# Kernel optimization log

Hardware: AMD Instinct MI355X
Metric: run time of the kernel (lower is better)

The kernel has to match this reference:

```python
import jax, jax.numpy as jnp
import numpy as np

PAD = 0  # padding token id; its embedding row is zero (padding_idx)


def setup_inputs() -> dict:
    key = jax.random.key(0)
    k1, k2, k3 = jax.random.split(key, 3)
    HOPS, VOCAB, D = 3, 50257, 128
    B, M, S = 32, 512, 6        # batch, memory slots, tokens per slot
    T, L = 128, 64              # trees per example, tokens per (flattened) tree
    # hop+1 embedding tables, normal(0, 0.1) like the torch init
    C = 0.1 * jax.random.normal(k1, (HOPS + 1, VOCAB, D), dtype=jnp.float32)
    C = C.at[:, PAD].set(0.0)   # padding_idx row = 0
    story = jax.random.randint(k2, (B, M, S), 0, VOCAB, dtype=jnp.int32)
    kb_tokens = jax.random.randint(k3, (B, T, L), 0, VOCAB, dtype=jnp.int32)
    return {"C": C, "story": story, "kb_tokens": kb_tokens}


def reference(C, story, kb_tokens):
    # C: [hops+1, V, D]; story: [B, M, S]; kb_tokens: [B, T, L]
    hops = C.shape[0] - 1
    B = story.shape[0]
    D = C.shape[-1]
    u = jnp.zeros((B, D), dtype=C.dtype)
    for hop in range(hops):
        # key memory: story slots (sum over tokens) + tree memories (sum over
        # all subtree tokens == dfs recursive sum, since PAD embeds to zero)
        m_story_A = jnp.take(C[hop], story, axis=0).sum(axis=2)       # [B,M,D]
        tree_A = jnp.take(C[hop], kb_tokens, axis=0).sum(axis=2)      # [B,T,D]
        m_A = jnp.concatenate([m_story_A, tree_A], axis=1)            # [B,M+T,D]
        prob = jax.nn.softmax(jnp.einsum("bmd,bd->bm", m_A, u), axis=1)
        # value memory with next-hop table
        m_story_C = jnp.take(C[hop + 1], story, axis=0).sum(axis=2)
        tree_C = jnp.take(C[hop + 1], kb_tokens, axis=0).sum(axis=2)
        m_C = jnp.concatenate([m_story_C, tree_C], axis=1)
        o_k = jnp.einsum("bm,bmd->bd", prob, m_C)
        u = u + o_k
    return u
```

## Files before the change

### kernel.cpp

```cpp
#include <hip/hip_runtime.h>
#include <math.h>

constexpr int HOPS  = 3;
constexpr int VOCAB = 50257;
constexpr int DIM   = 128;
constexpr int NB    = 32;
constexpr int NM    = 512;
constexpr int NS    = 6;
constexpr int NT    = 128;
constexpr int NL    = 64;
constexpr int SLOTS = NM + NT;
constexpr size_t TS = (size_t)VOCAB * DIM;
constexpr size_t TABSTRIDE = (size_t)NB * SLOTS * DIM;
constexpr int CHUNKS = SLOTS / 64;

constexpr size_t CH_ELEMS = (size_t)VOCAB * 3 * DIM;
constexpr int NE8 = (int)(CH_ELEMS / 8);

typedef _Float16 half8 __attribute__((ext_vector_type(8)));
typedef _Float16 half4 __attribute__((ext_vector_type(4)));

constexpr int CONV_BLOCKS  = 2048;
constexpr int STORY_BLOCKS = 2048;
constexpr int K1_BLOCKS    = CONV_BLOCKS + STORY_BLOCKS;
constexpr int TREE_BLOCKS  = NB * NT / 4;

__device__ __forceinline__ void addf4(float4& a, const float4& v) {
    a.x += v.x; a.y += v.y; a.z += v.z; a.w += v.w;
}

__global__ __launch_bounds__(256) void convert_story_k(
    const float* __restrict__ C, const int* __restrict__ story,
    _Float16* __restrict__ Ch, _Float16* __restrict__ msum)
{
    if (blockIdx.x & 1) {
        const int sb   = blockIdx.x >> 1;
        const int wave = threadIdx.x >> 6, lane = threadIdx.x & 63;
        const int h = lane >> 5, l32 = lane & 31;
        const int g = sb * 8 + wave * 2 + h;
        const int b = g >> 9, slot = g & (NM - 1);

        const int* idx = story + (size_t)g * NS;
        const int tokv = (l32 < NS) ? idx[l32] : 0;

        const float* Cb = C + TS + (size_t)l32 * 4;
        float4 a0 = {0,0,0,0}, a1 = {0,0,0,0}, a2 = {0,0,0,0};
        #pragma unroll
        for (int i = 0; i < NS; ++i) {
            const int s = __shfl(tokv, h * 32 + i);
            const float* p = Cb + (size_t)s * DIM;
            addf4(a0, *(const float4*)(p));
            addf4(a1, *(const float4*)(p + TS));
            addf4(a2, *(const float4*)(p + 2 * TS));
        }
        half4 h0, h1, h2;
        h0[0]=(_Float16)a0.x; h0[1]=(_Float16)a0.y; h0[2]=(_Float16)a0.z; h0[3]=(_Float16)a0.w;
        h1[0]=(_Float16)a1.x; h1[1]=(_Float16)a1.y; h1[2]=(_Float16)a1.z; h1[3]=(_Float16)a1.w;
        h2[0]=(_Float16)a2.x; h2[1]=(_Float16)a2.y; h2[2]=(_Float16)a2.z; h2[3]=(_Float16)a2.w;
        const size_t o = ((size_t)b * SLOTS + slot) * DIM + l32 * 4;
        *(half4*)(msum + o)                 = h0;
        *(half4*)(msum + o + TABSTRIDE)     = h1;
        *(half4*)(msum + o + 2 * TABSTRIDE) = h2;
    } else {
        const int cb = blockIdx.x >> 1;
        for (int e8 = cb * 256 + threadIdx.x; e8 < NE8; e8 += CONV_BLOCKS * 256) {
            const size_t base = (size_t)e8 * 8;
            const size_t v    = base / 384;
            const int    rem  = (int)(base % 384);
            const int    tab  = rem >> 7;
            const int    d    = rem & 127;
            const float* src = C + (size_t)(1 + tab) * TS + v * DIM + d;
            float4 f0 = *(const float4*)(src);
            float4 f1 = *(const float4*)(src + 4);
            half8 h;
            h[0]=(_Float16)f0.x; h[1]=(_Float16)f0.y; h[2]=(_Float16)f0.z; h[3]=(_Float16)f0.w;
            h[4]=(_Float16)f1.x; h[5]=(_Float16)f1.y; h[6]=(_Float16)f1.z; h[7]=(_Float16)f1.w;
            *(half8*)(Ch + base) = h;
        }
    }
}

__global__ __launch_bounds__(256) void tree_gather(
    const _Float16* __restrict__ Ch, const int* __restrict__ kb,
    _Float16* __restrict__ msum)
{
    const int wave = threadIdx.x >> 6, lane = threadIdx.x & 63;
    const int q = lane >> 4, l16 = lane & 15;
    const int g = blockIdx.x * 4 + wave;
    const int b = g >> 7, tr = g & (NT - 1);

    const int tok = kb[(size_t)g * NL + lane];

    float a0[8] = {0,0,0,0,0,0,0,0};
    float a1[8] = {0,0,0,0,0,0,0,0};
    float a2[8] = {0,0,0,0,0,0,0,0};

    #pragma unroll
    for (int i = 0; i < 16; ++i) {
        const int s = __shfl(tok, (lane & 48) + i);
        const _Float16* p = Ch + (size_t)s * (3 * DIM) + l16 * 8;
        half8 v0 = *(const half8*)(p);
        half8 v1 = *(const half8*)(p + DIM);
        half8 v2 = *(const half8*)(p + 2 * DIM);
        #pragma unroll
        for (int j = 0; j < 8; ++j) {
            a0[j] += (float)v0[j];
            a1[j] += (float)v1[j];
            a2[j] += (float)v2[j];
        }
    }
    #pragma unroll
    for (int j = 0; j < 8; ++j) {
        a0[j] += __shfl_xor(a0[j], 16); a0[j] += __shfl_xor(a0[j], 32);
        a1[j] += __shfl_xor(a1[j], 16); a1[j] += __shfl_xor(a1[j], 32);
        a2[j] += __shfl_xor(a2[j], 16); a2[j] += __shfl_xor(a2[j], 32);
    }
    if (q == 0) {
        half8 h0, h1, h2;
        #pragma unroll
        for (int j = 0; j < 8; ++j) {
            h0[j] = (_Float16)a0[j]; h1[j] = (_Float16)a1[j]; h2[j] = (_Float16)a2[j];
        }
        const size_t o = ((size_t)b * SLOTS + NM + tr) * DIM + l16 * 8;
        *(half8*)(msum + o)                 = h0;
        *(half8*)(msum + o + TABSTRIDE)     = h1;
        *(half8*)(msum + o + 2 * TABSTRIDE) = h2;
    }
}

__global__ __launch_bounds__(256) void hop0_k(
    const _Float16* __restrict__ msum, float* __restrict__ u)
{
    const int b = blockIdx.x, t = threadIdx.x, d = t & (DIM - 1), sub = t >> 7;
    const _Float16* mC = msum + ((size_t)b * SLOTS + sub * (SLOTS / 2)) * DIM + d;
    float acc = 0.f;
    #pragma unroll 16
    for (int m = 0; m < SLOTS / 2; ++m) acc += (float)mC[(size_t)m * DIM];
    __shared__ float red[256];
    red[t] = acc;
    __syncthreads();
    if (t < DIM) u[b * DIM + t] = (red[t] + red[t + 128]) * (1.f / SLOTS);
}

__device__ __forceinline__ float dot128h(const _Float16* __restrict__ row,
                                         const float* __restrict__ u_s)
{
    float acc = 0.f;
    const half8* r8 = (const half8*)row;
    #pragma unroll
    for (int i = 0; i < DIM / 8; ++i) {
        half8 h = r8[i];
        #pragma unroll
        for (int j = 0; j < 8; ++j) acc = fmaf((float)h[j], u_s[8 * i + j], acc);
    }
    return acc;
}

__global__ __launch_bounds__(256) void scores_softmax_k(
    const _Float16* __restrict__ msum, const float* __restrict__ u,
    float* __restrict__ sc, int tab)
{
    const int b = blockIdx.x, t = threadIdx.x, wv = t >> 6, ln = t & 63;
    __shared__ float u_s[DIM];
    __shared__ float red[4];
    if (t < DIM) u_s[t] = u[b * DIM + t];
    __syncthreads();

    const _Float16* mA = msum + (size_t)tab * TABSTRIDE + (size_t)b * SLOTS * DIM;
    float s0 = dot128h(mA + (size_t)t * DIM, u_s);
    float s1 = dot128h(mA + (size_t)(t + 256) * DIM, u_s);
    float s2 = (t < SLOTS - 512) ? dot128h(mA + (size_t)(t + 512) * DIM, u_s)
                                 : -INFINITY;

    float lmax = fmaxf(fmaxf(s0, s1), s2);
    #pragma unroll
    for (int off = 32; off > 0; off >>= 1) lmax = fmaxf(lmax, __shfl_xor(lmax, off));
    if (ln == 0) red[wv] = lmax;
    __syncthreads();
    lmax = fmaxf(fmaxf(red[0], red[1]), fmaxf(red[2], red[3]));
    __syncthreads();

    float e0 = expf(s0 - lmax), e1 = expf(s1 - lmax);
    float e2 = (t < SLOTS - 512) ? expf(s2 - lmax) : 0.f;
    float lsum = e0 + e1 + e2;
    #pragma unroll
    for (int off = 32; off > 0; off >>= 1) lsum += __shfl_xor(lsum, off);
    if (ln == 0) red[wv] = lsum;
    __syncthreads();
    const float inv = 1.0f / (red[0] + red[1] + red[2] + red[3]);

    float* s = sc + b * SLOTS;
    s[t] = e0 * inv;
    s[t + 256] = e1 * inv;
    if (t < SLOTS - 512) s[t + 512] = e2 * inv;
}

__global__ __launch_bounds__(256) void weighted_k(
    const _Float16* __restrict__ msum, const float* __restrict__ probs,
    float* __restrict__ u, int tab)
{
    const int b = blockIdx.x / CHUNKS, chunk = blockIdx.x % CHUNKS;
    const int t = threadIdx.x, d = t & (DIM - 1), sub = t >> 7;
    __shared__ float p[64];
    if (t < 64) p[t] = probs[b * SLOTS + chunk * 64 + t];
    __syncthreads();
    const _Float16* mC = msum + (size_t)tab * TABSTRIDE +
                         ((size_t)b * SLOTS + chunk * 64 + sub * 32) * DIM + d;
    float acc = 0.f;
    #pragma unroll
    for (int m = 0; m < 32; ++m)
        acc = fmaf(p[sub * 32 + m], (float)mC[(size_t)m * DIM], acc);
    __shared__ float red[256];
    red[t] = acc;
    __syncthreads();
    if (t < DIM) atomicAdd(&u[b * DIM + d], red[t] + red[t + 128]);
}

extern "C" void kernel_launch(void* const* d_in, const int* in_sizes, int n_in,
                              void* d_out, int out_size, void* d_ws, size_t ws_size,
                              hipStream_t stream) {
    const float* C     = (const float*)d_in[0];
    const int*   story = (const int*)d_in[1];
    const int*   kb    = (const int*)d_in[2];
    float*       u     = (float*)d_out;

    _Float16* Ch   = (_Float16*)d_ws;
    _Float16* msum = Ch + CH_ELEMS;
    float*    sc   = (float*)(msum + 3 * TABSTRIDE);

    convert_story_k<<<K1_BLOCKS, 256, 0, stream>>>(C, story, Ch, msum);
    tree_gather<<<TREE_BLOCKS, 256, 0, stream>>>(Ch, kb, msum);
    hop0_k<<<NB, 256, 0, stream>>>(msum , u);

    for (int hop = 1; hop < HOPS; ++hop) {
        scores_softmax_k<<<NB, 256, 0, stream>>>(msum, u, sc, hop - 1);
        weighted_k<<<NB * CHUNKS, 256, 0, stream>>>(msum, sc, u, hop);
    }
}
```

Before: 221.6 us.

## Fuse hop0, score/softmax and weighted-sum kernels into one per-batch kernel

Replaces the hop0, scores_softmax and weighted kernels (five launches) with a single kernel with one block per batch row. The block keeps u and the probabilities in shared memory and reads memory rows with 16-lane half8 vector loads, reducing dot products with shuffles. This removes several launches, the global probability buffer and the atomics, at the cost of running the weighted sum on only 32 blocks instead of 320, so less parallelism.

```diff
diff --git a/kernel.cpp b/kernel.cpp
--- a/kernel.cpp
+++ b/kernel.cpp
@@ -12,7 +12,6 @@
 constexpr int SLOTS = NM + NT;
 constexpr size_t TS = (size_t)VOCAB * DIM;
 constexpr size_t TABSTRIDE = (size_t)NB * SLOTS * DIM;
-constexpr int CHUNKS = SLOTS / 64;
 
 constexpr size_t CH_ELEMS = (size_t)VOCAB * 3 * DIM;
 constexpr int NE8 = (int)(CH_ELEMS / 8);
@@ -128,92 +127,92 @@
     }
 }
 
-__global__ __launch_bounds__(256) void hop0_k(
-    const _Float16* __restrict__ msum, float* __restrict__ u)
+__global__ __launch_bounds__(256) void hops_fused(
+    const _Float16* __restrict__ msum, float* __restrict__ out)
 {
-    const int b = blockIdx.x, t = threadIdx.x, d = t & (DIM - 1), sub = t >> 7;
-    const _Float16* mC = msum + ((size_t)b * SLOTS + sub * (SLOTS / 2)) * DIM + d;
-    float acc = 0.f;
-    #pragma unroll 16
-    for (int m = 0; m < SLOTS / 2; ++m) acc += (float)mC[(size_t)m * DIM];
-    __shared__ float red[256];
-    red[t] = acc;
-    __syncthreads();
-    if (t < DIM) u[b * DIM + t] = (red[t] + red[t + 128]) * (1.f / SLOTS);
-}
-
-__device__ __forceinline__ float dot128h(const _Float16* __restrict__ row,
-                                         const float* __restrict__ u_s)
-{
-    float acc = 0.f;
-    const half8* r8 = (const half8*)row;
-    #pragma unroll
-    for (int i = 0; i < DIM / 8; ++i) {
-        half8 h = r8[i];
-        #pragma unroll
-        for (int j = 0; j < 8; ++j) acc = fmaf((float)h[j], u_s[8 * i + j], acc);
-    }
-    return acc;
-}
-
-__global__ __launch_bounds__(256) void scores_softmax_k(
-    const _Float16* __restrict__ msum, const float* __restrict__ u,
-    float* __restrict__ sc, int tab)
-{
-    const int b = blockIdx.x, t = threadIdx.x, wv = t >> 6, ln = t & 63;
+    const int b = blockIdx.x, t = threadIdx.x;
+    const int rg = t >> 4, l16 = t & 15, wv = t >> 6, ln = t & 63;
     __shared__ float u_s[DIM];
+    __shared__ float probs[SLOTS];
+    __shared__ float part[16][DIM + 4];
     __shared__ float red[4];
-    if (t < DIM) u_s[t] = u[b * DIM + t];
-    __syncthreads();
-
-    const _Float16* mA = msum + (size_t)tab * TABSTRIDE + (size_t)b * SLOTS * DIM;
-    float s0 = dot128h(mA + (size_t)t * DIM, u_s);
-    float s1 = dot128h(mA + (size_t)(t + 256) * DIM, u_s);
-    float s2 = (t < SLOTS - 512) ? dot128h(mA + (size_t)(t + 512) * DIM, u_s)
-                                 : -INFINITY;
-
-    float lmax = fmaxf(fmaxf(s0, s1), s2);
-    #pragma unroll
-    for (int off = 32; off > 0; off >>= 1) lmax = fmaxf(lmax, __shfl_xor(lmax, off));
-    if (ln == 0) red[wv] = lmax;
-    __syncthreads();
-    lmax = fmaxf(fmaxf(red[0], red[1]), fmaxf(red[2], red[3]));
-    __syncthreads();
-
-    float e0 = expf(s0 - lmax), e1 = expf(s1 - lmax);
-    float e2 = (t < SLOTS - 512) ? expf(s2 - lmax) : 0.f;
-    float lsum = e0 + e1 + e2;
-    #pragma unroll
-    for (int off = 32; off > 0; off >>= 1) lsum += __shfl_xor(lsum, off);
-    if (ln == 0) red[wv] = lsum;
-    __syncthreads();
-    const float inv = 1.0f / (red[0] + red[1] + red[2] + red[3]);
-
-    float* s = sc + b * SLOTS;
-    s[t] = e0 * inv;
-    s[t + 256] = e1 * inv;
-    if (t < SLOTS - 512) s[t + 512] = e2 * inv;
-}
-
-__global__ __launch_bounds__(256) void weighted_k(
-    const _Float16* __restrict__ msum, const float* __restrict__ probs,
-    float* __restrict__ u, int tab)
-{
-    const int b = blockIdx.x / CHUNKS, chunk = blockIdx.x % CHUNKS;
-    const int t = threadIdx.x, d = t & (DIM - 1), sub = t >> 7;
-    __shared__ float p[64];
-    if (t < 64) p[t] = probs[b * SLOTS + chunk * 64 + t];
-    __syncthreads();
-    const _Float16* mC = msum + (size_t)tab * TABSTRIDE +
-                         ((size_t)b * SLOTS + chunk * 64 + sub * 32) * DIM + d;
-    float acc = 0.f;
-    #pragma unroll
-    for (int m = 0; m < 32; ++m)
-        acc = fmaf(p[sub * 32 + m], (float)mC[(size_t)m * DIM], acc);
-    __shared__ float red[256];
-    red[t] = acc;
-    __syncthreads();
-    if (t < DIM) atomicAdd(&u[b * DIM + d], red[t] + red[t + 128]);
+
+    const _Float16* base = msum + (size_t)b * SLOTS * DIM;
+
+    {
+        float acc[8] = {0,0,0,0,0,0,0,0};
+        for (int m = rg; m < SLOTS; m += 16) {
+            half8 v = *(const half8*)(base + (size_t)m * DIM + l16 * 8);
+            #pragma unroll
+            for (int j = 0; j < 8; ++j) acc[j] += (float)v[j];
+        }
+        #pragma unroll
+        for (int j = 0; j < 8; ++j) part[rg][l16 * 8 + j] = acc[j];
+        __syncthreads();
+        if (t < DIM) {
+            float s = 0.f;
+            #pragma unroll
+            for (int r = 0; r < 16; ++r) s += part[r][t];
+            u_s[t] = s * (1.f / SLOTS);
+        }
+        __syncthreads();
+    }
+
+    for (int hop = 1; hop < HOPS; ++hop) {
+        const _Float16* mA = base + (size_t)(hop - 1) * TABSTRIDE;
+        const _Float16* mC = base + (size_t)hop * TABSTRIDE;
+
+        for (int m = rg; m < SLOTS; m += 16) {
+            half8 v = *(const half8*)(mA + (size_t)m * DIM + l16 * 8);
+            float d = 0.f;
+            #pragma unroll
+            for (int j = 0; j < 8; ++j) d = fmaf((float)v[j], u_s[l16 * 8 + j], d);
+            d += __shfl_xor(d, 1); d += __shfl_xor(d, 2);
+            d += __shfl_xor(d, 4); d += __shfl_xor(d, 8);
+            if (l16 == 0) probs[m] = d;
+        }
+        __syncthreads();
+
+        float s0 = probs[t], s1 = probs[t + 256];
+        float s2 = (t < SLOTS - 512) ? probs[t + 512] : -INFINITY;
+        float lmax = fmaxf(fmaxf(s0, s1), s2);
+        #pragma unroll
+        for (int off = 32; off > 0; off >>= 1) lmax = fmaxf(lmax, __shfl_xor(lmax, off));
+        if (ln == 0) red[wv] = lmax;
+        __syncthreads();
+        lmax = fmaxf(fmaxf(red[0], red[1]), fmaxf(red[2], red[3]));
+        __syncthreads();
+        float e0 = expf(s0 - lmax), e1 = expf(s1 - lmax);
+        float e2 = (t < SLOTS - 512) ? expf(s2 - lmax) : 0.f;
+        probs[t] = e0; probs[t + 256] = e1;
+        if (t < SLOTS - 512) probs[t + 512] = e2;
+        float lsum = e0 + e1 + e2;
+        #pragma unroll
+        for (int off = 32; off > 0; off >>= 1) lsum += __shfl_xor(lsum, off);
+        if (ln == 0) red[wv] = lsum;
+        __syncthreads();
+        const float inv = 1.0f / (red[0] + red[1] + red[2] + red[3]);
+
+        float acc[8] = {0,0,0,0,0,0,0,0};
+        for (int m = rg; m < SLOTS; m += 16) {
+            const float p = probs[m];
+            half8 v = *(const half8*)(mC + (size_t)m * DIM + l16 * 8);
+            #pragma unroll
+            for (int j = 0; j < 8; ++j) acc[j] = fmaf(p, (float)v[j], acc[j]);
+        }
+        #pragma unroll
+        for (int j = 0; j < 8; ++j) part[rg][l16 * 8 + j] = acc[j];
+        __syncthreads();
+        if (t < DIM) {
+            float s = 0.f;
+            #pragma unroll
+            for (int r = 0; r < 16; ++r) s += part[r][t];
+            u_s[t] += s * inv;
+        }
+        __syncthreads();
+    }
+
+    if (t < DIM) out[b * DIM + t] = u_s[t];
 }
 
 extern "C" void kernel_launch(void* const* d_in, const int* in_sizes, int n_in,
@@ -222,18 +221,12 @@
     const float* C     = (const float*)d_in[0];
     const int*   story = (const int*)d_in[1];
     const int*   kb    = (const int*)d_in[2];
-    float*       u     = (float*)d_out;
+    float*       out   = (float*)d_out;
 
     _Float16* Ch   = (_Float16*)d_ws;
     _Float16* msum = Ch + CH_ELEMS;
-    float*    sc   = (float*)(msum + 3 * TABSTRIDE);
 
     convert_story_k<<<K1_BLOCKS, 256, 0, stream>>>(C, story, Ch, msum);
     tree_gather<<<TREE_BLOCKS, 256, 0, stream>>>(Ch, kb, msum);
-    hop0_k<<<NB, 256, 0, stream>>>(msum , u);
-
-    for (int hop = 1; hop < HOPS; ++hop) {
-        scores_softmax_k<<<NB, 256, 0, stream>>>(msum, u, sc, hop - 1);
-        weighted_k<<<NB * CHUNKS, 256, 0, stream>>>(msum, sc, u, hop);
-    }
-}
+    hops_fused<<<NB, 256, 0, stream>>>(msum, out);
+}
```

After: 251.3 us. 1.13x slower.
